# Optimization experiments

Measured on AMD Instinct MI355X. Metric: run time of the kernel, lower is better.

Reference implementation:

```python
import jax, jax.numpy as jnp
import numpy as np
from jax import lax


def _unfold(x, k, s):
    # torch.nn.functional.unfold: [B,C,H,W] -> [B, C*k*k, L], channel-major, row-major kernel offsets
    B, C, H, W = x.shape
    Ho = (H - k) // s + 1
    Wo = (W - k) // s + 1
    patches = [x[:, :, i:i + s * Ho:s, j:j + s * Wo:s] for i in range(k) for j in range(k)]
    stacked = jnp.stack(patches, axis=2)  # [B, C, k*k, Ho, Wo]
    return stacked.reshape(B, C * k * k, Ho * Wo)


def setup_inputs() -> dict:
    key = jax.random.key(0)
    x = jax.random.normal(key, (32, 69, 128, 128), dtype=jnp.float32)
    return {"x": x, "k": 2, "stride": 2}


def reference(x, k, stride):
    B, C, H, W = x.shape
    cs = C - 5  # number of pooled 'shape' channels
    # max pool over the first C-5 channels (kernel k, stride, no padding)
    pooled = lax.reduce_window(x[:, :cs], -jnp.inf, lax.max,
                               (1, 1, k, k), (1, 1, stride, stride), 'VALID')
    Ho, Wo = pooled.shape[2], pooled.shape[3]
    L = Ho * Wo
    kk = k * k
    # per-pixel L1 norm over channels, scaled
    shape_weights = jnp.sum(jnp.abs(x), axis=1, keepdims=True) / np.float32(np.sqrt(cs))
    sw = _unfold(shape_weights, k, stride)  # [B, kk, L]
    query = (sw / jnp.sum(jnp.abs(sw), axis=1, keepdims=True))[:, None]  # [B,1,kk,L]
    u_mean = _unfold(x[:, cs:cs + 2], k, stride).reshape(B, 2, kk, L)
    means = jnp.sum(u_mean * query, axis=2)  # [B,2,L]
    var1 = jnp.sum(_unfold(x[:, cs + 2:cs + 4], k, stride).reshape(B, 2, kk, L) * query, axis=2)
    var2 = jnp.sum((u_mean - means[:, :, None, :]) ** 2 * query, axis=2)
    window_var = var1 + var2
    cov1 = jnp.sum(_unfold(x[:, cs + 4:cs + 5], k, stride).reshape(B, 1, kk, L) * query, axis=2)
    cov2 = jnp.sum((u_mean[:, 0:1] - means[:, 0:1, None, :])
                   * (u_mean[:, 1:2] - means[:, 1:2, None, :])
                   * query ** 2, axis=2)
    window_covar = cov1 + cov2
    # cat + fold with (1,1) kernel == reshape to [B,5,Ho,Wo]
    agg = jnp.concatenate([means, window_var, window_covar], axis=1).reshape(B, 5, Ho, Wo)
    return jnp.concatenate([pooled, agg], axis=1)
```

## Files before the change

kernel.cpp:

```cpp
#include <hip/hip_runtime.h>

#define B_ 32
#define C_ 69
#define CS_ 64
#define H_ 128
#define W_ 128
#define HO_ 64
#define WO_ 64
#define HW_ (H_ * W_)
#define OHW_ (HO_ * WO_)

__global__ __launch_bounds__(256) void spatial_pool_kernel(
        const float* __restrict__ x, float* __restrict__ out) {
    const int lane = threadIdx.x & 63;
    const int w    = threadIdx.x >> 6;
    const int p    = lane & 31;
    const int rsel = lane >> 5;
    const int blk  = blockIdx.x;
    const int b    = blk >> 3;
    const int ho   = (blk & 7) * 8 + w * 2 + rsel;

    const float* xb = x   + (size_t)b * (C_ * HW_);
    float*       ob = out + (size_t)b * (C_ * OHW_);

    const int base0 = (2 * ho) * W_ + 4 * p;
    const int base1 = base0 + W_;
    const int opix  = ho * WO_ + 2 * p;

    float Sa0 = 0.f, Sa1 = 0.f, Sa2 = 0.f, Sa3 = 0.f;
    float Sb0 = 0.f, Sb1 = 0.f, Sb2 = 0.f, Sb3 = 0.f;

    #pragma unroll 4
    for (int c = 0; c < CS_; ++c) {
        const float* xc = xb + c * HW_;
        float4 r0 = *(const float4*)(xc + base0);
        float4 r1 = *(const float4*)(xc + base1);
        Sa0 += fabsf(r0.x); Sa1 += fabsf(r0.y);
        Sa2 += fabsf(r1.x); Sa3 += fabsf(r1.y);
        Sb0 += fabsf(r0.z); Sb1 += fabsf(r0.w);
        Sb2 += fabsf(r1.z); Sb3 += fabsf(r1.w);
        float2 m;
        m.x = fmaxf(fmaxf(r0.x, r0.y), fmaxf(r1.x, r1.y));
        m.y = fmaxf(fmaxf(r0.z, r0.w), fmaxf(r1.z, r1.w));
        *(float2*)(ob + c * OHW_ + opix) = m;
    }

    float4 t0[5], t1[5];
    #pragma unroll
    for (int d = 0; d < 5; ++d) {
        const float* xc = xb + (CS_ + d) * HW_;
        t0[d] = *(const float4*)(xc + base0);
        t1[d] = *(const float4*)(xc + base1);
        Sa0 += fabsf(t0[d].x); Sa1 += fabsf(t0[d].y);
        Sa2 += fabsf(t1[d].x); Sa3 += fabsf(t1[d].y);
        Sb0 += fabsf(t0[d].z); Sb1 += fabsf(t0[d].w);
        Sb2 += fabsf(t1[d].z); Sb3 += fabsf(t1[d].w);
    }

    float2 res[5];
    #pragma unroll
    for (int pix = 0; pix < 2; ++pix) {
        float q0, q1, q2, q3;
        float v64[4], v65[4], v66[4], v67[4], v68[4];
        if (pix == 0) {
            q0 = Sa0; q1 = Sa1; q2 = Sa2; q3 = Sa3;
            #pragma unroll
            for (int d = 0; d < 1; ++d) {}
            v64[0] = t0[0].x; v64[1] = t0[0].y; v64[2] = t1[0].x; v64[3] = t1[0].y;
            v65[0] = t0[1].x; v65[1] = t0[1].y; v65[2] = t1[1].x; v65[3] = t1[1].y;
            v66[0] = t0[2].x; v66[1] = t0[2].y; v66[2] = t1[2].x; v66[3] = t1[2].y;
            v67[0] = t0[3].x; v67[1] = t0[3].y; v67[2] = t1[3].x; v67[3] = t1[3].y;
            v68[0] = t0[4].x; v68[1] = t0[4].y; v68[2] = t1[4].x; v68[3] = t1[4].y;
        } else {
            q0 = Sb0; q1 = Sb1; q2 = Sb2; q3 = Sb3;
            v64[0] = t0[0].z; v64[1] = t0[0].w; v64[2] = t1[0].z; v64[3] = t1[0].w;
            v65[0] = t0[1].z; v65[1] = t0[1].w; v65[2] = t1[1].z; v65[3] = t1[1].w;
            v66[0] = t0[2].z; v66[1] = t0[2].w; v66[2] = t1[2].z; v66[3] = t1[2].w;
            v67[0] = t0[3].z; v67[1] = t0[3].w; v67[2] = t1[3].z; v67[3] = t1[3].w;
            v68[0] = t0[4].z; v68[1] = t0[4].w; v68[2] = t1[4].z; v68[3] = t1[4].w;
        }
        float inv = 1.0f / (q0 + q1 + q2 + q3);
        float q[4] = {q0 * inv, q1 * inv, q2 * inv, q3 * inv};

        float m0 = 0.f, m1 = 0.f;
        #pragma unroll
        for (int j = 0; j < 4; ++j) {
            m0 += v64[j] * q[j];
            m1 += v65[j] * q[j];
        }
        float vv0 = 0.f, vv1 = 0.f, cv = 0.f;
        #pragma unroll
        for (int j = 0; j < 4; ++j) {
            float d0 = v64[j] - m0;
            float d1 = v65[j] - m1;
            vv0 += v66[j] * q[j] + d0 * d0 * q[j];
            vv1 += v67[j] * q[j] + d1 * d1 * q[j];
            cv  += v68[j] * q[j] + d0 * d1 * q[j] * q[j];
        }
        if (pix == 0) {
            res[0].x = m0; res[1].x = m1; res[2].x = vv0; res[3].x = vv1; res[4].x = cv;
        } else {
            res[0].y = m0; res[1].y = m1; res[2].y = vv0; res[3].y = vv1; res[4].y = cv;
        }
    }

    #pragma unroll
    for (int d = 0; d < 5; ++d)
        *(float2*)(ob + (CS_ + d) * OHW_ + opix) = res[d];
}

extern "C" void kernel_launch(void* const* d_in, const int* in_sizes, int n_in,
                              void* d_out, int out_size, void* d_ws, size_t ws_size,
                              hipStream_t stream) {
    const float* x = (const float*)d_in[0];
    float* out = (float*)d_out;
    const int grid = B_ * (HO_ / 8);
    spatial_pool_kernel<<<grid, 256, 0, stream>>>(x, out);
}
```

Before: 214.8 us.

## Batch channel loads in groups of 32 with nontemporal access and staggered channel order

Restructures the channel loop into two fully unrolled groups of 32 channels. All loads in a group are issued before the pooled maxima are written, and each block uses a per-block rotated channel order to spread DRAM channel/bank traffic. Loads and stores now use nontemporal builtins to avoid polluting caches on streaming data. This raises memory-level parallelism at the cost of much higher register pressure (32 float2 maxima plus 64 in-flight float4 loads), which may reduce occupancy.

```diff
diff --git a/kernel.cpp b/kernel.cpp
--- a/kernel.cpp
+++ b/kernel.cpp
@@ -9,6 +9,9 @@
 #define WO_ 64
 #define HW_ (H_ * W_)
 #define OHW_ (HO_ * WO_)
+
+typedef float f32x4 __attribute__((ext_vector_type(4)));
+typedef float f32x2 __attribute__((ext_vector_type(2)));
 
 __global__ __launch_bounds__(256) void spatial_pool_kernel(
         const float* __restrict__ x, float* __restrict__ out) {
@@ -26,46 +29,52 @@
     const int base0 = (2 * ho) * W_ + 4 * p;
     const int base1 = base0 + W_;
     const int opix  = ho * WO_ + 2 * p;
+    const int off   = (blk * 11) & 31;
 
     float Sa0 = 0.f, Sa1 = 0.f, Sa2 = 0.f, Sa3 = 0.f;
     float Sb0 = 0.f, Sb1 = 0.f, Sb2 = 0.f, Sb3 = 0.f;
 
-    #pragma unroll 4
-    for (int c = 0; c < CS_; ++c) {
-        const float* xc = xb + c * HW_;
-        float4 r0 = *(const float4*)(xc + base0);
-        float4 r1 = *(const float4*)(xc + base1);
-        Sa0 += fabsf(r0.x); Sa1 += fabsf(r0.y);
-        Sa2 += fabsf(r1.x); Sa3 += fabsf(r1.y);
-        Sb0 += fabsf(r0.z); Sb1 += fabsf(r0.w);
-        Sb2 += fabsf(r1.z); Sb3 += fabsf(r1.w);
-        float2 m;
-        m.x = fmaxf(fmaxf(r0.x, r0.y), fmaxf(r1.x, r1.y));
-        m.y = fmaxf(fmaxf(r0.z, r0.w), fmaxf(r1.z, r1.w));
-        *(float2*)(ob + c * OHW_ + opix) = m;
+    for (int g = 0; g < 2; ++g) {
+        f32x2 mx[32];
+        #pragma unroll
+        for (int i = 0; i < 32; ++i) {
+            const int c = g * 32 + ((i + off) & 31);
+            const float* xc = xb + c * HW_;
+            f32x4 r0 = __builtin_nontemporal_load((const f32x4*)(xc + base0));
+            f32x4 r1 = __builtin_nontemporal_load((const f32x4*)(xc + base1));
+            Sa0 += fabsf(r0.x); Sa1 += fabsf(r0.y);
+            Sa2 += fabsf(r1.x); Sa3 += fabsf(r1.y);
+            Sb0 += fabsf(r0.z); Sb1 += fabsf(r0.w);
+            Sb2 += fabsf(r1.z); Sb3 += fabsf(r1.w);
+            mx[i].x = fmaxf(fmaxf(r0.x, r0.y), fmaxf(r1.x, r1.y));
+            mx[i].y = fmaxf(fmaxf(r0.z, r0.w), fmaxf(r1.z, r1.w));
+        }
+        #pragma unroll
+        for (int i = 0; i < 32; ++i) {
+            const int c = g * 32 + ((i + off) & 31);
+            __builtin_nontemporal_store(mx[i], (f32x2*)(ob + c * OHW_ + opix));
+        }
     }
 
-    float4 t0[5], t1[5];
+    f32x4 t0[5], t1[5];
     #pragma unroll
     for (int d = 0; d < 5; ++d) {
         const float* xc = xb + (CS_ + d) * HW_;
-        t0[d] = *(const float4*)(xc + base0);
-        t1[d] = *(const float4*)(xc + base1);
+        t0[d] = __builtin_nontemporal_load((const f32x4*)(xc + base0));
+        t1[d] = __builtin_nontemporal_load((const f32x4*)(xc + base1));
         Sa0 += fabsf(t0[d].x); Sa1 += fabsf(t0[d].y);
         Sa2 += fabsf(t1[d].x); Sa3 += fabsf(t1[d].y);
         Sb0 += fabsf(t0[d].z); Sb1 += fabsf(t0[d].w);
         Sb2 += fabsf(t1[d].z); Sb3 += fabsf(t1[d].w);
     }
 
-    float2 res[5];
+    f32x2 res[5];
     #pragma unroll
     for (int pix = 0; pix < 2; ++pix) {
         float q0, q1, q2, q3;
         float v64[4], v65[4], v66[4], v67[4], v68[4];
         if (pix == 0) {
             q0 = Sa0; q1 = Sa1; q2 = Sa2; q3 = Sa3;
-            #pragma unroll
-            for (int d = 0; d < 1; ++d) {}
             v64[0] = t0[0].x; v64[1] = t0[0].y; v64[2] = t1[0].x; v64[3] = t1[0].y;
             v65[0] = t0[1].x; v65[1] = t0[1].y; v65[2] = t1[1].x; v65[3] = t1[1].y;
             v66[0] = t0[2].x; v66[1] = t0[2].y; v66[2] = t1[2].x; v66[3] = t1[2].y;
@@ -106,7 +115,7 @@
 
     #pragma unroll
     for (int d = 0; d < 5; ++d)
-        *(float2*)(ob + (CS_ + d) * OHW_ + opix) = res[d];
+        __builtin_nontemporal_store(res[d], (f32x2*)(ob + (CS_ + d) * OHW_ + opix));
 }
 
 extern "C" void kernel_launch(void* const* d_in, const int* in_sizes, int n_in,
```

New measurement: 215.1 us. No clear change (+0.1%).
